# Kernel optimization log

Hardware: AMD Instinct MI355X
Metric: run time of the kernel (lower is better)

## Reference

```python
import jax, jax.numpy as jnp
import numpy as np

EPS_LN = 1e-5
EPS_NORM = 1e-12
TEMP = 0.07

def _layernorm(x, g, b):
    m = jnp.mean(x, axis=-1, keepdims=True)
    v = jnp.var(x, axis=-1, keepdims=True)
    return (x - m) * jax.lax.rsqrt(v + EPS_LN) * g + b

def _l2norm(x):
    n = jnp.linalg.norm(x, axis=-1, keepdims=True)
    return x / jnp.maximum(n, EPS_NORM)

def setup_inputs() -> dict:
    key = jax.random.key(0)
    ks = jax.random.split(key, 8)
    B, N, Df, Dp, K = 64, 4096, 384, 256, 8
    H = W = 64
    def w(k, shp, scale):
        return jax.random.normal(k, shp, jnp.float32) * scale
    return {
        "patch_features": jax.random.normal(ks[0], (B, N, Df), jnp.float32),
        "H": H, "W": W,
        "W_proj": w(ks[1], (Df, Dp), 0.03), "b_proj": jnp.zeros((Dp,), jnp.float32),
        "g1": jnp.ones((Dp,), jnp.float32), "beta1": jnp.zeros((Dp,), jnp.float32),
        "prototypes": w(ks[2], (K, Dp), 0.02),
        "g2": jnp.ones((Dp,), jnp.float32), "beta2": jnp.zeros((Dp,), jnp.float32),
        "W_r1": w(ks[3], (Dp, 2 * Dp), 0.03), "b_r1": jnp.zeros((2 * Dp,), jnp.float32),
        "W_r2": w(ks[4], (2 * Dp, Dp), 0.03), "b_r2": jnp.zeros((Dp,), jnp.float32),
        "W_s1": w(ks[5], (Dp, 64), 0.05), "b_s1": jnp.zeros((64,), jnp.float32),
        "W_s2": w(ks[6], (64, 1), 0.05), "b_s2": jnp.zeros((1,), jnp.float32),
    }

def reference(patch_features, H, W, W_proj, b_proj, g1, beta1, prototypes,
              g2, beta2, W_r1, b_r1, W_r2, b_r2, W_s1, b_s1, W_s2, b_s2):
    gelu = lambda x: jax.nn.gelu(x, approximate=False)  # torch exact GELU
    # feat_proj: Linear -> LayerNorm -> GELU   [B,N,Dp]
    feat = gelu(_layernorm(patch_features @ W_proj + b_proj, g1, beta1))
    feat_norm = _l2norm(feat)
    proto_norm = _l2norm(prototypes)
    sim = jnp.einsum('bnd,kd->bnk', feat_norm, proto_norm) / TEMP
    assign = jax.nn.softmax(sim, axis=-1)            # [B,N,K]
    mass = jnp.clip(assign.sum(axis=1), 1e-6, None)[:, :, None]  # [B,K,1]
    part_feat = jnp.einsum('bnk,bnd->bkd', assign, feat) / mass  # [B,K,Dp]
    # refine MLP: LN -> Linear(2Dp) -> GELU -> Linear(Dp), residual add
    h = _layernorm(part_feat, g2, beta2)
    part_feat = part_feat + (gelu(h @ W_r1 + b_r1) @ W_r2 + b_r2)
    # normalized grid coordinates [N,2] = (x, y)
    gy = jnp.arange(H, dtype=jnp.float32) / max(H - 1, 1)
    gx = jnp.arange(W, dtype=jnp.float32) / max(W - 1, 1)
    grid_y, grid_x = jnp.meshgrid(gy, gx, indexing='ij')
    coords = jnp.stack([grid_x.reshape(-1), grid_y.reshape(-1)], axis=-1)
    part_pos = jnp.einsum('bnk,nc->bkc', assign, coords) / mass  # [B,K,2]
    salience = jax.nn.sigmoid(gelu(part_feat @ W_s1 + b_s1) @ W_s2 + b_s2)[..., 0]
    return (part_feat, part_pos, assign, salience, feat)
```

## Files before the change

kernel.cpp:

```cpp
#include <hip/hip_runtime.h>
#include <hip/hip_bf16.h>
#include <stdint.h>
#include <stddef.h>

#define DF 384
#define DP 256
#define NPROT 8
#define NPB 4096
#define KSTEPS 12

typedef __attribute__((ext_vector_type(8))) short bf16x8;
typedef __attribute__((ext_vector_type(4))) short bf16x4;
typedef __attribute__((ext_vector_type(4))) float f32x4;

typedef const __attribute__((address_space(1))) unsigned char as1_u8;
typedef __attribute__((address_space(3))) unsigned char as3_u8;

static __device__ __forceinline__ short f2bf(float f) {
  __hip_bfloat16 h(f);
  return *reinterpret_cast<short*>(&h);
}
static __device__ __forceinline__ float gelu_f(float x) {
  float x3 = x * x * x;
  float t = __expf(1.5957691216057308f * fmaf(0.044715f, x3, x));
  return x - x / (t + 1.0f);
}

static __device__ __forceinline__ f32x4 mfma16x16x16_bf16(bf16x4 a, bf16x4 b, f32x4 c) {
#if __has_builtin(__builtin_amdgcn_mfma_f32_16x16x16bf16_1k)
  return __builtin_amdgcn_mfma_f32_16x16x16bf16_1k(a, b, c, 0, 0, 0);
#else
  asm volatile("v_mfma_f32_16x16x16_bf16 %0, %1, %2, %0" : "+v"(c) : "v"(a), "v"(b));
  return c;
#endif
}

__global__ __launch_bounds__(256) void k_setup(const float* __restrict__ W,
                                               unsigned short* __restrict__ wT,
                                               const float* __restrict__ P,
                                               float* __restrict__ PN,
                                               unsigned short* __restrict__ pb) {
  if (blockIdx.x < 384) {
    int e = blockIdx.x * 256 + threadIdx.x;
    int c = e / DF;
    int k = e - c * DF;
    wT[e] = (unsigned short)f2bf(W[k * DP + c]);
  } else {
    __shared__ float s_red[4];
    __shared__ float s_pn[NPROT][DP];
    const int tid = threadIdx.x;
    const int lane = tid & 63, wave = tid >> 6;
    for (int r = 0; r < NPROT; r++) {
      float x = P[r * DP + tid];
      float q = x * x;
      #pragma unroll
      for (int d = 1; d < 64; d <<= 1) q += __shfl_xor(q, d);
      if (lane == 0) s_red[wave] = q;
      __syncthreads();
      float ss = s_red[0] + s_red[1] + s_red[2] + s_red[3];
      float v = x / fmaxf(sqrtf(ss), 1e-12f);
      PN[r * DP + tid] = v;
      s_pn[r][tid] = v;
      __syncthreads();
    }
    for (int i = tid; i < 512; i += 256) {
      int step = i >> 6, l = i & 63;
      int k = l & 15, g = l >> 4;
      bf16x8 v;
      #pragma unroll
      for (int j = 0; j < 8; j++) {
        int d = step * 32 + g * 8 + j;
        v[j] = (k < NPROT) ? f2bf(s_pn[k][d]) : (short)0;
      }
      *(bf16x8*)(pb + (size_t)i * 8) = v;
    }
  }
}

__global__ __launch_bounds__(256, 3) void k_fused(
    const float* __restrict__ patch,
    const float* __restrict__ bias,
    const float* __restrict__ g1,
    const float* __restrict__ beta1,
    const unsigned short* __restrict__ wT,
    const unsigned short* __restrict__ pb,
    float* __restrict__ out_feat,
    float* __restrict__ out_assign,
    float* __restrict__ part_partial,
    float* __restrict__ mp_partial,
    float* __restrict__ acc_part,
    float* __restrict__ acc_mass,
    float* __restrict__ acc_pos,
    int use_part) {
  __shared__ __align__(16) unsigned char Bbuf[33792];
  __shared__ __align__(16) unsigned short s_pb[512 * 8];
  __shared__ float s_bias[DP], s_g1[DP], s_b1[DP];
  __shared__ float s_mp[4][3][NPROT];

  const int tid  = threadIdx.x;
  const int lane = tid & 63;
  const int wave = tid >> 6;
  const int mrow = lane & 15;
  const int kgrp = lane >> 4;

  const long long row0 = (long long)blockIdx.x * 64;
  const int b  = (int)(row0 >> 12);
  const int n0 = (int)(row0 & 4095);

  s_bias[tid] = bias[tid];
  s_g1[tid]   = g1[tid];
  s_b1[tid]   = beta1[tid];
  *(bf16x8*)(s_pb + (size_t)tid * 8)         = *(const bf16x8*)(pb + (size_t)tid * 8);
  *(bf16x8*)(s_pb + (size_t)(256 + tid) * 8) = *(const bf16x8*)(pb + (size_t)(256 + tid) * 8);

  const float* arow = patch + (size_t)(row0 + wave * 16 + mrow) * DF + kgrp * 8;
  bf16x8 afrag[KSTEPS];
  #pragma unroll
  for (int kt = 0; kt < KSTEPS; kt++) {
    float4 x0 = *(const float4*)(arow + kt * 32);
    float4 x1 = *(const float4*)(arow + kt * 32 + 4);
    bf16x8 a;
    a[0] = f2bf(x0.x); a[1] = f2bf(x0.y); a[2] = f2bf(x0.z); a[3] = f2bf(x0.w);
    a[4] = f2bf(x1.x); a[5] = f2bf(x1.y); a[6] = f2bf(x1.z); a[7] = f2bf(x1.w);
    afrag[kt] = a;
  }

  f32x4 acc[16];
  #pragma unroll
  for (int f = 0; f < 16; f++) acc[f] = (f32x4){0.f, 0.f, 0.f, 0.f};

  #define STAGE(kt_, q_)                                                        \
    {                                                                           \
      _Pragma("unroll")                                                         \
      for (int i = 0; i < 4; i++) {                                             \
        int e   = i * 256 + tid;                                                \
        int col = e >> 2;                                                       \
        int t4  = e & 3;                                                        \
        int sub = t4 ^ ((col >> 1) & 3);                                        \
        const unsigned short* src = wT + col * DF + (kt_) * 32 + sub * 8;       \
        int lofs = __builtin_amdgcn_readfirstlane(                              \
            (q_) * 16384 + (i * 256 + wave * 64) * 16);                         \
        __builtin_amdgcn_global_load_lds((as1_u8*)(const void*)src,             \
                                         (as3_u8*)(void*)(Bbuf + lofs), 16, 0, 0); \
      }                                                                         \
    }

  STAGE(0, 0);
  __syncthreads();

  const int lane_swz = mrow * 64 + (kgrp ^ ((mrow >> 1) & 3)) * 16;

  #pragma unroll
  for (int kt = 0; kt < KSTEPS; kt++) {
    if (kt + 1 < KSTEPS) STAGE(kt + 1, (kt + 1) & 1);
    if (kt > 0) {
      if (kt + 1 < KSTEPS) asm volatile("s_waitcnt vmcnt(4)" ::: "memory");
      else                 asm volatile("s_waitcnt vmcnt(0)" ::: "memory");
      __builtin_amdgcn_s_barrier();
      __builtin_amdgcn_sched_barrier(0);
    }
    const unsigned char* bbase = Bbuf + (kt & 1) * 16384 + lane_swz;
    bf16x8 a = afrag[kt];
    #pragma unroll
    for (int f = 0; f < 16; f++) {
      bf16x8 bf = *(const bf16x8*)(bbase + f * 1024);
      acc[f] = __builtin_amdgcn_mfma_f32_16x16x32_bf16(a, bf, acc[f], 0, 0, 0);
    }
    asm volatile("s_waitcnt lgkmcnt(0)" ::: "memory");
    __builtin_amdgcn_s_barrier();
    __builtin_amdgcn_sched_barrier(0);
  }
  #undef STAGE

  #pragma unroll
  for (int f = 0; f < 16; f++) {
    const float bb = s_bias[f * 16 + mrow];
    #pragma unroll
    for (int r = 0; r < 4; r++) acc[f][r] += bb;
  }
  #pragma unroll
  for (int r = 0; r < 4; r++) {
    float s = 0.f, q = 0.f;
    #pragma unroll
    for (int f = 0; f < 16; f++) { float x = acc[f][r]; s += x; q += x * x; }
    #pragma unroll
    for (int d = 1; d < 16; d <<= 1) { s += __shfl_xor(s, d); q += __shfl_xor(q, d); }
    const float mean = s * (1.f / 256.f);
    const float var  = q * (1.f / 256.f) - mean * mean;
    const float rstd = rsqrtf(var + 1e-5f);
    #pragma unroll
    for (int f = 0; f < 16; f++) {
      const int col = f * 16 + mrow;
      float y = (acc[f][r] - mean) * rstd * s_g1[col] + s_b1[col];
      acc[f][r] = gelu_f(y);
    }
  }

  float ssn[4];
  #pragma unroll
  for (int r = 0; r < 4; r++) {
    float q2 = 0.f;
    #pragma unroll
    for (int f = 0; f < 16; f++) q2 += acc[f][r] * acc[f][r];
    #pragma unroll
    for (int d = 1; d < 16; d <<= 1) q2 += __shfl_xor(q2, d);
    ssn[r] = q2;
  }

  f32x4 cdot = (f32x4){0.f, 0.f, 0.f, 0.f};
  {
    float* s_tr = (float*)Bbuf;
    const int rr = lane >> 5;
    const int cc = (lane & 31) * 4;
    float* fb = out_feat + (size_t)(row0 + wave * 16) * DP;
    const int aoff = (wave * 16 + mrow) * 132 + kgrp * 8;
    #pragma unroll
    for (int p = 0; p < 2; p++) {
      #pragma unroll
      for (int fl = 0; fl < 8; fl++) {
        const int f = 8 * p + fl;
        #pragma unroll
        for (int r = 0; r < 4; r++)
          s_tr[(wave * 16 + kgrp * 4 + r) * 132 + fl * 16 + mrow] = acc[f][r];
      }
      #pragma unroll
      for (int i = 0; i < 8; i++) {
        const int row = i * 2 + rr;
        f32x4 v = *(const f32x4*)&s_tr[(wave * 16 + row) * 132 + cc];
        *(f32x4*)&fb[(size_t)row * DP + p * 128 + cc] = v;
      }
      #pragma unroll
      for (int s = 0; s < 4; s++) {
        float4 y0 = *(const float4*)&s_tr[aoff + s * 32];
        float4 y1 = *(const float4*)&s_tr[aoff + s * 32 + 4];
        bf16x8 a;
        a[0] = f2bf(y0.x); a[1] = f2bf(y0.y); a[2] = f2bf(y0.z); a[3] = f2bf(y0.w);
        a[4] = f2bf(y1.x); a[5] = f2bf(y1.y); a[6] = f2bf(y1.z); a[7] = f2bf(y1.w);
        bf16x8 pf = *(const bf16x8*)(s_pb + (size_t)((p * 4 + s) * 64 + lane) * 8);
        cdot = __builtin_amdgcn_mfma_f32_16x16x32_bf16(a, pf, cdot, 0, 0, 0);
      }
    }
  }

  float asg[4];
  #pragma unroll
  for (int r = 0; r < 4; r++) {
    const float nrm = fmaxf(sqrtf(ssn[r]), 1e-12f);
    float lg = (mrow < NPROT) ? (cdot[r] / nrm) * (1.f / 0.07f) : -1e30f;
    float mx = lg;
    #pragma unroll
    for (int d = 1; d < 16; d <<= 1) mx = fmaxf(mx, __shfl_xor(mx, d));
    float e = __expf(lg - mx);
    float se = e;
    #pragma unroll
    for (int d = 1; d < 16; d <<= 1) se += __shfl_xor(se, d);
    asg[r] = e / se;
  }

  float pm = 0.f, px = 0.f, py = 0.f;
  #pragma unroll
  for (int r = 0; r < 4; r++) {
    const int n = n0 + wave * 16 + kgrp * 4 + r;
    if (mrow < NPROT)
      out_assign[((size_t)b * NPB + n) * NPROT + mrow] = asg[r];
    const float cx = (float)(n & 63) * (1.f / 63.f);
    const float cy = (float)(n >> 6) * (1.f / 63.f);
    pm += asg[r]; px += asg[r] * cx; py += asg[r] * cy;
  }
  pm += __shfl_xor(pm, 16); pm += __shfl_xor(pm, 32);
  px += __shfl_xor(px, 16); px += __shfl_xor(px, 32);
  py += __shfl_xor(py, 16); py += __shfl_xor(py, 32);
  if (lane < NPROT) {
    s_mp[wave][0][lane] = pm;
    s_mp[wave][1][lane] = px;
    s_mp[wave][2][lane] = py;
  }

  __syncthreads();

  {
    float* s_partw = (float*)Bbuf;
    bf16x4 a4;
    #pragma unroll
    for (int j = 0; j < 4; j++) a4[j] = f2bf(asg[j]);
    #pragma unroll
    for (int f = 0; f < 16; f++) {
      bf16x4 b4;
      #pragma unroll
      for (int j = 0; j < 4; j++) b4[j] = f2bf(acc[f][j]);
      f32x4 c = mfma16x16x16_bf16(a4, b4, (f32x4){0.f, 0.f, 0.f, 0.f});
      if (kgrp < 2) {
        #pragma unroll
        for (int r = 0; r < 4; r++)
          s_partw[((wave * 8 + kgrp * 4 + r)) * 256 + f * 16 + mrow] = c[r];
      }
    }
  }
  __syncthreads();

  {
    const float* s_partw = (const float*)Bbuf;
    float pr[NPROT];
    #pragma unroll
    for (int k = 0; k < NPROT; k++)
      pr[k] = s_partw[(0 * 8 + k) * 256 + tid] + s_partw[(1 * 8 + k) * 256 + tid] +
              s_partw[(2 * 8 + k) * 256 + tid] + s_partw[(3 * 8 + k) * 256 + tid];

    if (use_part) {
      float* pp = part_partial + (size_t)blockIdx.x * 2048;
      #pragma unroll
      for (int k = 0; k < NPROT; k++) pp[k * 256 + tid] = pr[k];
      if (tid < 24) {
        const int v = tid >> 3, k = tid & 7;
        float s = s_mp[0][v][k] + s_mp[1][v][k] + s_mp[2][v][k] + s_mp[3][v][k];
        mp_partial[(size_t)blockIdx.x * 32 + v * 8 + k] = s;
      }
    } else {
      float* gp = acc_part + (size_t)b * (NPROT * DP);
      #pragma unroll
      for (int k = 0; k < NPROT; k++) atomicAdd(&gp[k * 256 + tid], pr[k]);
      if (tid < 24) {
        const int v = tid >> 3, k = tid & 7;
        float s = s_mp[0][v][k] + s_mp[1][v][k] + s_mp[2][v][k] + s_mp[3][v][k];
        if (v == 0) atomicAdd(&acc_mass[b * NPROT + k], s);
        else        atomicAdd(&acc_pos[(b * NPROT + k) * 2 + (v - 1)], s);
      }
    }
  }
}

__global__ __launch_bounds__(256) void k_reduce(const float* __restrict__ pp,
                                                float* __restrict__ acc_part) {
  const int b = blockIdx.x >> 3;
  const int j = blockIdx.x & 7;
  const int col = j * 256 + threadIdx.x;
  const float* base = pp + (size_t)b * 64 * 2048 + col;
  float a0 = 0.f, a1 = 0.f, a2 = 0.f, a3 = 0.f;
  #pragma unroll
  for (int p = 0; p < 64; p += 4) {
    a0 += base[(size_t)p * 2048];
    a1 += base[(size_t)(p + 1) * 2048];
    a2 += base[(size_t)(p + 2) * 2048];
    a3 += base[(size_t)(p + 3) * 2048];
  }
  acc_part[(size_t)b * 2048 + col] = (a0 + a1) + (a2 + a3);
}

__global__ __launch_bounds__(256) void k_final(
    const float* __restrict__ mp_partial,
    const float* __restrict__ acc_part, const float* __restrict__ acc_mass,
    const float* __restrict__ acc_pos,
    const float* __restrict__ g2, const float* __restrict__ beta2,
    const float* __restrict__ W_r1, const float* __restrict__ b_r1,
    const float* __restrict__ W_r2, const float* __restrict__ b_r2,
    const float* __restrict__ W_s1, const float* __restrict__ b_s1,
    const float* __restrict__ W_s2, const float* __restrict__ b_s2,
    float* __restrict__ out_pf, float* __restrict__ out_pos, float* __restrict__ out_sal,
    int use_part) {
  __shared__ float s_pf[8 * DP];
  __shared__ float s_h[8 * DP];
  __shared__ float s_t[8 * 512];
  __shared__ float s_pff[8 * DP];
  __shared__ float s_s1v[8 * 64];
  __shared__ float s_m[8];
  __shared__ float s_red[8];
  const int b = blockIdx.x;
  const int tid = threadIdx.x;
  const int lane = tid & 63, wave = tid >> 6;

  if (use_part) {
    if (tid < 8) {
      float m = 0.f, x = 0.f, y = 0.f;
      for (int j = 0; j < 64; j++) {
        const float* q = mp_partial + ((size_t)b * 64 + j) * 32;
        m += q[tid]; x += q[8 + tid]; y += q[16 + tid];
      }
      m = fmaxf(m, 1e-6f);
      s_m[tid] = m;
      out_pos[b * 16 + tid * 2 + 0] = x / m;
      out_pos[b * 16 + tid * 2 + 1] = y / m;
    }
  } else {
    if (tid < 8) s_m[tid] = fmaxf(acc_mass[b * 8 + tid], 1e-6f);
    if (tid >= 64 && tid < 80) {
      int t = tid - 64;
      out_pos[b * 16 + t] = acc_pos[b * 16 + t] / fmaxf(acc_mass[b * 8 + (t >> 1)], 1e-6f);
    }
  }
  __syncthreads();
  #pragma unroll
  for (int i = 0; i < 8; i++) {
    int idx = i * 256 + tid;
    s_pf[idx] = acc_part[(size_t)b * 2048 + idx] / s_m[i];
  }
  __syncthreads();

  for (int r = 0; r < 8; r++) {
    float x = s_pf[r * DP + tid];
    float s = x, q = x * x;
    #pragma unroll
    for (int d = 1; d < 64; d <<= 1) { s += __shfl_xor(s, d); q += __shfl_xor(q, d); }
    if (lane == 0) { s_red[wave] = s; s_red[4 + wave] = q; }
    __syncthreads();
    float ts = s_red[0] + s_red[1] + s_red[2] + s_red[3];
    float tq = s_red[4] + s_red[5] + s_red[6] + s_red[7];
    float mean = ts * (1.f / 256.f);
    float var  = tq * (1.f / 256.f) - mean * mean;
    s_h[r * DP + tid] = (x - mean) * rsqrtf(var + 1e-5f) * g2[tid] + beta2[tid];
    __syncthreads();
  }

  #pragma unroll
  for (int i = 0; i < 2; i++) {
    const int o = i * 256 + tid;
    float a[8];
    #pragma unroll
    for (int r = 0; r < 8; r++) a[r] = 0.f;
    #pragma unroll 8
    for (int c = 0; c < DP; c++) {
      const float w = W_r1[c * 512 + o];
      #pragma unroll
      for (int r = 0; r < 8; r++) a[r] += s_h[r * DP + c] * w;
    }
    const float bb = b_r1[o];
    #pragma unroll
    for (int r = 0; r < 8; r++) s_t[r * 512 + o] = gelu_f(a[r] + bb);
  }
  __syncthreads();

  {
    const int o = tid;
    float a[8];
    #pragma unroll
    for (int r = 0; r < 8; r++) a[r] = 0.f;
    #pragma unroll 8
    for (int c = 0; c < 512; c++) {
      const float w = W_r2[c * DP + o];
      #pragma unroll
      for (int r = 0; r < 8; r++) a[r] += s_t[r * 512 + c] * w;
    }
    const float bb = b_r2[o];
    #pragma unroll
    for (int r = 0; r < 8; r++) {
      float v = s_pf[r * DP + o] + a[r] + bb;
      s_pff[r * DP + o] = v;
      out_pf[(size_t)b * 2048 + r * DP + o] = v;
    }
  }
  __syncthreads();

  if (tid < 64) {
    const int o = tid;
    float a[8];
    #pragma unroll
    for (int r = 0; r < 8; r++) a[r] = 0.f;
    #pragma unroll 8
    for (int c = 0; c < DP; c++) {
      const float w = W_s1[c * 64 + o];
      #pragma unroll
      for (int r = 0; r < 8; r++) a[r] += s_pff[r * DP + c] * w;
    }
    const float bb = b_s1[o];
    #pragma unroll
    for (int r = 0; r < 8; r++) s_s1v[r * 64 + o] = gelu_f(a[r] + bb);
  }
  __syncthreads();

  if (tid < 8) {
    float a = 0.f;
    for (int c = 0; c < 64; c++) a += s_s1v[tid * 64 + c] * W_s2[c];
    a += b_s2[0];
    out_sal[b * 8 + tid] = 1.f / (1.f + __expf(-a));
  }
}

extern "C" void kernel_launch(void* const* d_in, const int* in_sizes, int n_in,
                              void* d_out, int out_size, void* d_ws, size_t ws_size,
                              hipStream_t stream) {
  (void)in_sizes; (void)n_in; (void)out_size;
  const float* patch  = (const float*)d_in[0];
  const float* W_proj = (const float*)d_in[3];
  const float* b_proj = (const float*)d_in[4];
  const float* g1     = (const float*)d_in[5];
  const float* beta1  = (const float*)d_in[6];
  const float* proto  = (const float*)d_in[7];
  const float* g2     = (const float*)d_in[8];
  const float* beta2  = (const float*)d_in[9];
  const float* W_r1   = (const float*)d_in[10];
  const float* b_r1   = (const float*)d_in[11];
  const float* W_r2   = (const float*)d_in[12];
  const float* b_r2   = (const float*)d_in[13];
  const float* W_s1   = (const float*)d_in[14];
  const float* b_s1   = (const float*)d_in[15];
  const float* W_s2   = (const float*)d_in[16];
  const float* b_s2   = (const float*)d_in[17];

  float* out = (float*)d_out;
  float* out_pf     = out;
  float* out_pos    = out + 131072;
  float* out_assign = out + 132096;
  float* out_sal    = out + 2229248;
  float* out_feat   = out + 2229760;

  char* ws = (char*)d_ws;
  unsigned short* wT  = (unsigned short*)ws;
  float* protoN       = (float*)(ws + 196608);
  unsigned short* pbf = (unsigned short*)(ws + 204800);
  float* acc_part     = (float*)(ws + 262144);
  float* acc_mass     = (float*)(ws + 786432);
  float* acc_pos      = (float*)(ws + 788480);
  float* part_partial = (float*)(ws + 1048576);
  float* mp_partial   = (float*)(ws + 1048576 + 33554432);

  const size_t need_part = 1048576ull + 33554432ull + 524288ull;
  const int use_part = (ws_size >= need_part) ? 1 : 0;

  if (!use_part) hipMemsetAsync(ws + 262144, 0, 530432, stream);
  k_setup<<<385, 256, 0, stream>>>(W_proj, wT, proto, protoN, pbf);
  k_fused<<<4096, 256, 0, stream>>>(patch, b_proj, g1, beta1, wT, pbf,
                                    out_feat, out_assign,
                                    part_partial, mp_partial,
                                    acc_part, acc_mass, acc_pos, use_part);
  if (use_part) k_reduce<<<512, 256, 0, stream>>>(part_partial, acc_part);
  k_final<<<64, 256, 0, stream>>>(mp_partial, acc_part, acc_mass, acc_pos,
                                  g2, beta2, W_r1, b_r1, W_r2, b_r2,
                                  W_s1, b_s1, W_s2, b_s2,
                                  out_pf, out_pos, out_sal, use_part);
}
```

Measured before the change: 327.3 us.

## Stream A fragments per k-step and drop LDS prototype copy for higher occupancy

```diff
diff --git a/kernel.cpp b/kernel.cpp
--- a/kernel.cpp
+++ b/kernel.cpp
@@ -77,7 +77,7 @@
   }
 }
 
-__global__ __launch_bounds__(256, 3) void k_fused(
+__global__ __launch_bounds__(256, 4) void k_fused(
     const float* __restrict__ patch,
     const float* __restrict__ bias,
     const float* __restrict__ g1,
@@ -93,7 +93,6 @@
     float* __restrict__ acc_pos,
     int use_part) {
   __shared__ __align__(16) unsigned char Bbuf[33792];
-  __shared__ __align__(16) unsigned short s_pb[512 * 8];
   __shared__ float s_bias[DP], s_g1[DP], s_b1[DP];
   __shared__ float s_mp[4][3][NPROT];
 
@@ -110,24 +109,6 @@
   s_bias[tid] = bias[tid];
   s_g1[tid]   = g1[tid];
   s_b1[tid]   = beta1[tid];
-  *(bf16x8*)(s_pb + (size_t)tid * 8)         = *(const bf16x8*)(pb + (size_t)tid * 8);
-  *(bf16x8*)(s_pb + (size_t)(256 + tid) * 8) = *(const bf16x8*)(pb + (size_t)(256 + tid) * 8);
-
-  const float* arow = patch + (size_t)(row0 + wave * 16 + mrow) * DF + kgrp * 8;
-  bf16x8 afrag[KSTEPS];
-  #pragma unroll
-  for (int kt = 0; kt < KSTEPS; kt++) {
-    float4 x0 = *(const float4*)(arow + kt * 32);
-    float4 x1 = *(const float4*)(arow + kt * 32 + 4);
-    bf16x8 a;
-    a[0] = f2bf(x0.x); a[1] = f2bf(x0.y); a[2] = f2bf(x0.z); a[3] = f2bf(x0.w);
-    a[4] = f2bf(x1.x); a[5] = f2bf(x1.y); a[6] = f2bf(x1.z); a[7] = f2bf(x1.w);
-    afrag[kt] = a;
-  }
-
-  f32x4 acc[16];
-  #pragma unroll
-  for (int f = 0; f < 16; f++) acc[f] = (f32x4){0.f, 0.f, 0.f, 0.f};
 
   #define STAGE(kt_, q_)                                                        \
     {                                                                           \
@@ -145,22 +126,34 @@
       }                                                                         \
     }
 
+  const float* arow = patch + (size_t)(row0 + wave * 16 + mrow) * DF + kgrp * 8;
+  float4 a0c = *(const float4*)(arow);
+  float4 a1c = *(const float4*)(arow + 4);
   STAGE(0, 0);
-  __syncthreads();
+
+  f32x4 acc[16];
+  #pragma unroll
+  for (int f = 0; f < 16; f++) acc[f] = (f32x4){0.f, 0.f, 0.f, 0.f};
 
   const int lane_swz = mrow * 64 + (kgrp ^ ((mrow >> 1) & 3)) * 16;
 
   #pragma unroll
   for (int kt = 0; kt < KSTEPS; kt++) {
-    if (kt + 1 < KSTEPS) STAGE(kt + 1, (kt + 1) & 1);
-    if (kt > 0) {
-      if (kt + 1 < KSTEPS) asm volatile("s_waitcnt vmcnt(4)" ::: "memory");
-      else                 asm volatile("s_waitcnt vmcnt(0)" ::: "memory");
-      __builtin_amdgcn_s_barrier();
-      __builtin_amdgcn_sched_barrier(0);
-    }
+    float4 a0n, a1n;
+    if (kt + 1 < KSTEPS) {
+      a0n = *(const float4*)(arow + (kt + 1) * 32);
+      a1n = *(const float4*)(arow + (kt + 1) * 32 + 4);
+      STAGE(kt + 1, (kt + 1) & 1);
+      asm volatile("s_waitcnt vmcnt(6)" ::: "memory");
+    } else {
+      asm volatile("s_waitcnt vmcnt(0)" ::: "memory");
+    }
+    __builtin_amdgcn_s_barrier();
+    __builtin_amdgcn_sched_barrier(0);
+    bf16x8 a;
+    a[0] = f2bf(a0c.x); a[1] = f2bf(a0c.y); a[2] = f2bf(a0c.z); a[3] = f2bf(a0c.w);
+    a[4] = f2bf(a1c.x); a[5] = f2bf(a1c.y); a[6] = f2bf(a1c.z); a[7] = f2bf(a1c.w);
     const unsigned char* bbase = Bbuf + (kt & 1) * 16384 + lane_swz;
-    bf16x8 a = afrag[kt];
     #pragma unroll
     for (int f = 0; f < 16; f++) {
       bf16x8 bf = *(const bf16x8*)(bbase + f * 1024);
@@ -169,6 +162,7 @@
     asm volatile("s_waitcnt lgkmcnt(0)" ::: "memory");
     __builtin_amdgcn_s_barrier();
     __builtin_amdgcn_sched_barrier(0);
+    if (kt + 1 < KSTEPS) { a0c = a0n; a1c = a1n; }
   }
   #undef STAGE
 
@@ -236,7 +230,7 @@
         bf16x8 a;
         a[0] = f2bf(y0.x); a[1] = f2bf(y0.y); a[2] = f2bf(y0.z); a[3] = f2bf(y0.w);
         a[4] = f2bf(y1.x); a[5] = f2bf(y1.y); a[6] = f2bf(y1.z); a[7] = f2bf(y1.w);
-        bf16x8 pf = *(const bf16x8*)(s_pb + (size_t)((p * 4 + s) * 64 + lane) * 8);
+        bf16x8 pf = *(const bf16x8*)(pb + (size_t)((p * 4 + s) * 64 + lane) * 8);
         cdot = __builtin_amdgcn_mfma_f32_16x16x32_bf16(a, pf, cdot, 0, 0, 0);
       }
     }
```

Result: slower. 500.3 us (+52.9%).
